# Kernel tuning notes

Hardware: AMD Instinct MI355X
Metric: run time of the kernel (lower is better)

## Reference

```python
import jax, jax.numpy as jnp
import numpy as np
from jax import lax

IN_C, OUT_C, K, Z_DIM, STRIDE = 128, 128, 3, 256, 1


def setup_inputs() -> dict:
    key = jax.random.key(0)
    k1, k2, k3, k4, k5 = jax.random.split(key, 5)
    B, H, W = 16, 64, 64
    x = jax.random.normal(k1, (B, IN_C, H, W), dtype=jnp.float32)
    z = jax.random.normal(k2, (B, Z_DIM), dtype=jnp.float32)
    # base conv weight, He-style init as in the torch module
    base_weight = jax.random.normal(k3, (OUT_C, IN_C, K, K), dtype=jnp.float32) * (2.0 / (IN_C * K * K)) ** 0.5
    # delta_weight_head: nn.Linear(z_dim, out_c*in_c*k*k) -> weight [out_dim, z_dim], bias [out_dim]
    out_dim = OUT_C * IN_C * K * K
    lim = 1.0 / np.sqrt(Z_DIM)
    head_w = jax.random.uniform(k4, (out_dim, Z_DIM), dtype=jnp.float32, minval=-lim, maxval=lim)
    head_b = jax.random.uniform(k5, (out_dim,), dtype=jnp.float32, minval=-lim, maxval=lim)
    return {"x": x, "z": z, "base_weight": base_weight, "head_w": head_w, "head_b": head_b}


def reference(x, z, base_weight, head_w, head_b):
    B = x.shape[0]
    # per-sample weight deltas: [B, out_c*in_c*k*k] -> [B, out_c, in_c, k, k]
    delta_w = (z @ head_w.T + head_b).reshape(B, OUT_C, IN_C, K, K)
    w = base_weight[None] + delta_w  # [B, out_c, in_c, k, k]
    pad = K // 2

    def conv_one(xb, wb):
        # xb: [in_c, H, W], wb: [out_c, in_c, k, k]
        return lax.conv_general_dilated(
            xb[None], wb, window_strides=(STRIDE, STRIDE),
            padding=[(pad, pad), (pad, pad)],
            dimension_numbers=("NCHW", "OIHW", "NCHW"))[0]

    out = jax.vmap(conv_one)(x, w)  # [B, out_c, H_out, W_out]
    return out
```

## Files before the change

kernel.cpp:

```cpp
#include <hip/hip_runtime.h>
#include <hip/hip_bf16.h>
#include <cstdint>
#include <cstddef>

typedef _Float16 f16;
typedef _Float16 f16x8 __attribute__((ext_vector_type(8)));
typedef float f32x4 __attribute__((ext_vector_type(4)));

#define BATCH 16
#define INC   128
#define OUTC  128
#define HH    64
#define WW    64
#define HP    66
#define WP    66
#define ZDIM  256

#define XP_ELEMS (16ull * HP * WP * INC)
#define WA_ELEMS (16ull * 9 * OUTC * INC)

__global__ __launch_bounds__(256) void zero_xp(f16* __restrict__ xp) {
    size_t i = (size_t)blockIdx.x * 256 + threadIdx.x;
    uint4 zv = {0u, 0u, 0u, 0u};
    *(uint4*)(xp + i * 8) = zv;
}

__global__ __launch_bounds__(256) void xprep(const float* __restrict__ x,
                                             f16* __restrict__ xp) {
    int blk = blockIdx.x;
    int icC = blk & 3;
    int h   = (blk >> 2) & 63;
    int b   = blk >> 8;
    int ic0 = icC * 32;
    int tid = threadIdx.x;

    __shared__ float tile[32 * 65];

    {
        int i = tid >> 3;
        int j = tid & 7;
        const float4* src = (const float4*)(x + (((size_t)b * INC + ic0 + i) * HH + h) * WW) + j * 2;
        float4 v0 = src[0];
        float4 v1 = src[1];
        float* tp = tile + i * 65 + j * 8;
        tp[0] = v0.x; tp[1] = v0.y; tp[2] = v0.z; tp[3] = v0.w;
        tp[4] = v1.x; tp[5] = v1.y; tp[6] = v1.z; tp[7] = v1.w;
    }
    __syncthreads();
    {
        int w = tid >> 2;
        int q = tid & 3;
        f16 o8[8];
#pragma unroll
        for (int jj = 0; jj < 8; ++jj)
            o8[jj] = (f16)tile[(q * 8 + jj) * 65 + w];
        f16* dst = xp + (((size_t)b * HP + (h + 1)) * WP + (w + 1)) * INC + ic0 + q * 8;
        *(uint4*)dst = *(uint4*)o8;
    }
}

__device__ inline f16x8 cvt8(float4 a, float4 b) {
    f16x8 r;
    r[0] = (f16)a.x; r[1] = (f16)a.y; r[2] = (f16)a.z; r[3] = (f16)a.w;
    r[4] = (f16)b.x; r[5] = (f16)b.y; r[6] = (f16)b.z; r[7] = (f16)b.w;
    return r;
}

__global__ __launch_bounds__(256) void wgen(const float* __restrict__ z,
                                            const float* __restrict__ base_w,
                                            const float* __restrict__ head_w,
                                            const float* __restrict__ head_b,
                                            f16* __restrict__ wA) {
    int tid  = threadIdx.x;
    int lane = tid & 63;
    int wv   = tid >> 6;
    int r16  = lane & 15;
    int quad = lane >> 4;
    int row0 = (blockIdx.x * 4 + wv) * 16;
    int myrow = row0 + r16;

    const float4* zrow = (const float4*)(z + (size_t)r16 * ZDIM);
    f16x8 bfr[8];
#pragma unroll
    for (int s = 0; s < 8; ++s) {
        float4 z0 = zrow[s * 8 + quad * 2];
        float4 z1 = zrow[s * 8 + quad * 2 + 1];
        bfr[s] = cvt8(z0, z1);
    }

    const float4* hw = (const float4*)(head_w + (size_t)myrow * ZDIM);
    f32x4 acc = {0.f, 0.f, 0.f, 0.f};
#pragma unroll
    for (int s = 0; s < 8; ++s) {
        float4 a0 = hw[s * 8 + quad * 2];
        float4 a1 = hw[s * 8 + quad * 2 + 1];
        acc = __builtin_amdgcn_mfma_f32_16x16x32_f16(cvt8(a0, a1), bfr[s], acc, 0, 0, 0);
    }

#pragma unroll
    for (int reg = 0; reg < 4; ++reg) {
        int o = row0 + quad * 4 + reg;
        float cst = base_w[o] + head_b[o];
        int r  = o % 9;
        int oc = o / 1152;
        int ic = (o / 9) % 128;
        wA[(size_t)r16 * (9 * OUTC * INC) + ((size_t)r * OUTC + oc) * INC + ic] =
            (f16)(cst + acc[reg]);
    }
}

__global__ __launch_bounds__(256) void conv(const f16* __restrict__ xp,
                                            const f16* __restrict__ wA,
                                            float* __restrict__ out) {
    int blk = blockIdx.x;
    int b  = blk >> 5;
    int pt = blk & 31;
    int h0 = pt * 2;

    int tid   = threadIdx.x;
    int lane  = tid & 63;
    int wv    = tid >> 6;
    int ocHalf = wv & 1;
    int pHalf  = wv >> 1;
    int m0    = ocHalf * 64;
    int row16 = lane & 15;
    int quad  = lane >> 4;

    __shared__ __align__(16) f16 ws3[3 * 128 * 40];
    __shared__ __align__(16) f16 xs[2 * 66 * 40];

    f32x4 acc[4][4];
#pragma unroll
    for (int mt = 0; mt < 4; ++mt)
#pragma unroll
        for (int nt = 0; nt < 4; ++nt)
            acc[mt][nt] = f32x4{0.f, 0.f, 0.f, 0.f};

    for (int c = 0; c < 4; ++c) {
        int ic0 = c * 32;
#pragma unroll
        for (int kh = 0; kh < 3; ++kh) {
            __syncthreads();
#pragma unroll
            for (int i = 0; i < 6; ++i) {
                int idx  = tid + i * 256;
                int seg  = idx >> 2;
                int part = idx & 3;
                int kw = seg >> 7;
                int oc = seg & 127;
                const uint4* src = (const uint4*)(wA +
                    ((((size_t)b * 9 + kh * 3 + kw) * OUTC + oc) * INC + ic0)) + part;
                *(uint4*)(ws3 + (kw * 128 + oc) * 40 + part * 8) = *src;
            }
            for (int idx = tid; idx < 528; idx += 256) {
                int seg  = idx >> 2;
                int part = idx & 3;
                int row  = seg / 66;
                int wc   = seg - row * 66;
                const uint4* src = (const uint4*)(xp +
                    (((size_t)b * HP + h0 + kh + row) * WP + wc) * INC + ic0) + part;
                *(uint4*)(xs + (row * 66 + wc) * 40 + part * 8) = *src;
            }
            __syncthreads();
#pragma unroll
            for (int kw = 0; kw < 3; ++kw) {
                f16x8 afr[4], bfr[4];
#pragma unroll
                for (int mt = 0; mt < 4; ++mt)
                    afr[mt] = *(const f16x8*)(ws3 + ((kw * 128 + m0 + mt * 16 + row16) * 40 + quad * 8));
#pragma unroll
                for (int nt = 0; nt < 4; ++nt)
                    bfr[nt] = *(const f16x8*)(xs + ((pHalf * 66 + nt * 16 + row16 + kw) * 40 + quad * 8));
#pragma unroll
                for (int mt = 0; mt < 4; ++mt)
#pragma unroll
                    for (int nt = 0; nt < 4; ++nt)
                        acc[mt][nt] = __builtin_amdgcn_mfma_f32_16x16x32_f16(
                            afr[mt], bfr[nt], acc[mt][nt], 0, 0, 0);
            }
        }
    }

    int hrow = h0 + pHalf;
#pragma unroll
    for (int mt = 0; mt < 4; ++mt)
#pragma unroll
        for (int nt = 0; nt < 4; ++nt) {
            int wc = nt * 16 + row16;
#pragma unroll
            for (int reg = 0; reg < 4; ++reg) {
                int oc = m0 + mt * 16 + quad * 4 + reg;
                out[(((size_t)b * OUTC + oc) * HH + hrow) * WW + wc] = acc[mt][nt][reg];
            }
        }
}

extern "C" void kernel_launch(void* const* d_in, const int* in_sizes, int n_in,
                              void* d_out, int out_size, void* d_ws, size_t ws_size,
                              hipStream_t stream) {
    const float* x      = (const float*)d_in[0];
    const float* z      = (const float*)d_in[1];
    const float* base_w = (const float*)d_in[2];
    const float* head_w = (const float*)d_in[3];
    const float* head_b = (const float*)d_in[4];
    float* out = (float*)d_out;

    f16* xp = (f16*)d_ws;
    f16* wAp = xp + XP_ELEMS;

    zero_xp<<<(unsigned)(XP_ELEMS / 8 / 256), 256, 0, stream>>>(xp);
    xprep  <<<16 * 64 * 4, 256, 0, stream>>>(x, xp);
    wgen   <<<(OUTC * INC * 9) / 64, 256, 0, stream>>>(z, base_w, head_w,
                                                       head_b, wAp);
    conv   <<<16 * 32, 256, 0, stream>>>(xp, wAp, out);
}
```

Measured before the change: 302.1 us.

## Zero only padding border, remap wgen tiles for coalesced stores, stage 4 input rows once

The padding kernel now writes zeros only to the border rows and columns of the padded input, since the interior is overwritten by xprep anyway. The weight-generation kernel remaps its tiles so each lane stores four contiguous fp16 input-channel weights, replacing the previous scattered 2-byte stores. It also software-pipelines its head_w loads. The conv kernel loads all four padded input rows for each channel chunk once, instead of reloading two rows for every kh, which cuts global-to-LDS traffic at the cost of more shared memory.

After: 288.7 us. 1.05x faster.

```diff
diff --git a/kernel.cpp b/kernel.cpp
--- a/kernel.cpp
+++ b/kernel.cpp
@@ -5,6 +5,7 @@
 
 typedef _Float16 f16;
 typedef _Float16 f16x8 __attribute__((ext_vector_type(8)));
+typedef _Float16 f16x4 __attribute__((ext_vector_type(4)));
 typedef float f32x4 __attribute__((ext_vector_type(4)));
 
 #define BATCH 16
@@ -20,9 +21,24 @@
 #define WA_ELEMS (16ull * 9 * OUTC * INC)
 
 __global__ __launch_bounds__(256) void zero_xp(f16* __restrict__ xp) {
-    size_t i = (size_t)blockIdx.x * 256 + threadIdx.x;
+    unsigned i = blockIdx.x * 256 + threadIdx.x;
+    unsigned b = i / 4160;
+    unsigned j = i - b * 4160;
+    unsigned row, wc, ic8;
+    if (j < 2112) {
+        row = (j < 1056) ? 0u : 65u;
+        unsigned jj = (j < 1056) ? j : j - 1056;
+        wc  = jj >> 4;
+        ic8 = jj & 15;
+    } else {
+        unsigned j2 = j - 2112;
+        row = 1 + (j2 >> 5);
+        unsigned k = j2 & 31;
+        wc  = (k < 16) ? 0u : 65u;
+        ic8 = k & 15;
+    }
     uint4 zv = {0u, 0u, 0u, 0u};
-    *(uint4*)(xp + i * 8) = zv;
+    *(uint4*)(xp + (((size_t)b * HP + row) * WP + wc) * INC + ic8 * 8) = zv;
 }
 
 __global__ __launch_bounds__(256) void xprep(const float* __restrict__ x,
@@ -76,37 +92,43 @@
     int wv   = tid >> 6;
     int r16  = lane & 15;
     int quad = lane >> 4;
-    int row0 = (blockIdx.x * 4 + wv) * 16;
-    int myrow = row0 + r16;
+    int tile = blockIdx.x * 4 + wv;
+    int icb  = tile & 7;
+    int oc   = (tile >> 3) & 127;
+    int r    = tile >> 10;
+    int base = (oc * 128 + icb * 16) * 9 + r;
+    int myrow = base + 9 * r16;
 
     const float4* zrow = (const float4*)(z + (size_t)r16 * ZDIM);
     f16x8 bfr[8];
 #pragma unroll
+    for (int s = 0; s < 8; ++s)
+        bfr[s] = cvt8(zrow[s * 8 + quad * 2], zrow[s * 8 + quad * 2 + 1]);
+
+    const float4* hw = (const float4*)(head_w + (size_t)myrow * ZDIM);
+    float4 a[3][2];
+    a[0][0] = hw[quad * 2];     a[0][1] = hw[quad * 2 + 1];
+    a[1][0] = hw[8 + quad * 2]; a[1][1] = hw[8 + quad * 2 + 1];
+    f32x4 acc = {0.f, 0.f, 0.f, 0.f};
+#pragma unroll
     for (int s = 0; s < 8; ++s) {
-        float4 z0 = zrow[s * 8 + quad * 2];
-        float4 z1 = zrow[s * 8 + quad * 2 + 1];
-        bfr[s] = cvt8(z0, z1);
-    }
-
-    const float4* hw = (const float4*)(head_w + (size_t)myrow * ZDIM);
-    f32x4 acc = {0.f, 0.f, 0.f, 0.f};
-#pragma unroll
-    for (int s = 0; s < 8; ++s) {
-        float4 a0 = hw[s * 8 + quad * 2];
-        float4 a1 = hw[s * 8 + quad * 2 + 1];
-        acc = __builtin_amdgcn_mfma_f32_16x16x32_f16(cvt8(a0, a1), bfr[s], acc, 0, 0, 0);
-    }
-
+        if (s + 2 < 8) {
+            a[(s + 2) % 3][0] = hw[(s + 2) * 8 + quad * 2];
+            a[(s + 2) % 3][1] = hw[(s + 2) * 8 + quad * 2 + 1];
+        }
+        acc = __builtin_amdgcn_mfma_f32_16x16x32_f16(
+            cvt8(a[s % 3][0], a[s % 3][1]), bfr[s], acc, 0, 0, 0);
+    }
+
+    f16x4 ov;
+    int icl = quad * 4;
 #pragma unroll
     for (int reg = 0; reg < 4; ++reg) {
-        int o = row0 + quad * 4 + reg;
-        float cst = base_w[o] + head_b[o];
-        int r  = o % 9;
-        int oc = o / 1152;
-        int ic = (o / 9) % 128;
-        wA[(size_t)r16 * (9 * OUTC * INC) + ((size_t)r * OUTC + oc) * INC + ic] =
-            (f16)(cst + acc[reg]);
-    }
+        int o = base + 9 * (icl + reg);
+        ov[reg] = (f16)(base_w[o] + head_b[o] + acc[reg]);
+    }
+    size_t idx = (((size_t)r16 * 9 + r) * OUTC + oc) * INC + icb * 16 + icl;
+    *(f16x4*)(wA + idx) = ov;
 }
 
 __global__ __launch_bounds__(256) void conv(const f16* __restrict__ xp,
@@ -127,7 +149,7 @@
     int quad  = lane >> 4;
 
     __shared__ __align__(16) f16 ws3[3 * 128 * 40];
-    __shared__ __align__(16) f16 xs[2 * 66 * 40];
+    __shared__ __align__(16) f16 xs[4 * 66 * 40];
 
     f32x4 acc[4][4];
 #pragma unroll
@@ -152,14 +174,16 @@
                     ((((size_t)b * 9 + kh * 3 + kw) * OUTC + oc) * INC + ic0)) + part;
                 *(uint4*)(ws3 + (kw * 128 + oc) * 40 + part * 8) = *src;
             }
-            for (int idx = tid; idx < 528; idx += 256) {
-                int seg  = idx >> 2;
-                int part = idx & 3;
-                int row  = seg / 66;
-                int wc   = seg - row * 66;
-                const uint4* src = (const uint4*)(xp +
-                    (((size_t)b * HP + h0 + kh + row) * WP + wc) * INC + ic0) + part;
-                *(uint4*)(xs + (row * 66 + wc) * 40 + part * 8) = *src;
+            if (kh == 0) {
+                for (int idx = tid; idx < 1056; idx += 256) {
+                    int seg  = idx >> 2;
+                    int part = idx & 3;
+                    int row  = seg / 66;
+                    int wc   = seg - row * 66;
+                    const uint4* src = (const uint4*)(xp +
+                        (((size_t)b * HP + h0 + row) * WP + wc) * INC + ic0) + part;
+                    *(uint4*)(xs + (row * 66 + wc) * 40 + part * 8) = *src;
+                }
             }
             __syncthreads();
 #pragma unroll
@@ -170,7 +194,7 @@
                     afr[mt] = *(const f16x8*)(ws3 + ((kw * 128 + m0 + mt * 16 + row16) * 40 + quad * 8));
 #pragma unroll
                 for (int nt = 0; nt < 4; ++nt)
-                    bfr[nt] = *(const f16x8*)(xs + ((pHalf * 66 + nt * 16 + row16 + kw) * 40 + quad * 8));
+                    bfr[nt] = *(const f16x8*)(xs + (((kh + pHalf) * 66 + nt * 16 + row16 + kw) * 40 + quad * 8));
 #pragma unroll
                 for (int mt = 0; mt < 4; ++mt)
 #pragma unroll
@@ -208,7 +232,7 @@
     f16* xp = (f16*)d_ws;
     f16* wAp = xp + XP_ELEMS;
 
-    zero_xp<<<(unsigned)(XP_ELEMS / 8 / 256), 256, 0, stream>>>(xp);
+    zero_xp<<<260, 256, 0, stream>>>(xp);
     xprep  <<<16 * 64 * 4, 256, 0, stream>>>(x, xp);
     wgen   <<<(OUTC * INC * 9) / 64, 256, 0, stream>>>(z, base_w, head_w,
                                                        head_b, wAp);
```
